# Kernel tuning notes

Hardware: AMD Instinct MI355X
Metric: run time of the kernel (lower is better)

## Reference

```python
import jax, jax.numpy as jnp
import numpy as np

DECAY = 0.99
EPS = 1e-05


def setup_inputs() -> dict:
    key = jax.random.key(0)
    k1, k2 = jax.random.split(key)
    B, C, H, W = 16, 64, 32, 32
    K = 8192
    z_e = jax.random.normal(k1, (B, C, H, W), dtype=jnp.float32)
    embedding = jax.random.normal(k2, (K, C), dtype=jnp.float32)
    cluster_size = jnp.zeros((K,), dtype=jnp.float32)
    embedding_avg = embedding  # initialized as a clone of the codebook
    return {"z_e": z_e, "embedding": embedding, "cluster_size": cluster_size,
            "embedding_avg": embedding_avg}


def reference(z_e, embedding, cluster_size, embedding_avg):
    B, C, H, W = z_e.shape
    K = embedding.shape[0]
    # [N, C] tokens
    z_flat = jnp.transpose(z_e, (0, 2, 3, 1)).reshape(-1, C)
    d = ((z_flat * z_flat).sum(-1, keepdims=True)
         - 2.0 * (z_flat @ embedding.T)
         + (embedding * embedding).sum(-1))
    indices = jnp.argmin(d, axis=1)  # [N] int
    z_q_flat = embedding[indices]    # [N, C]
    z_q = jnp.transpose(z_q_flat.reshape(B, H, W, C), (0, 3, 1, 2))
    # EMA codebook update (training path); one-hot matmuls expressed as segment sums
    counts = jax.ops.segment_sum(jnp.ones(z_flat.shape[0], dtype=z_flat.dtype),
                                 indices, num_segments=K)            # encodings.sum(0)
    dw = jax.ops.segment_sum(z_flat, indices, num_segments=K)        # encodings.T @ z_flat
    new_cluster_size = DECAY * cluster_size + (1.0 - DECAY) * counts
    new_embedding_avg = DECAY * embedding_avg + (1.0 - DECAY) * dw
    n = new_cluster_size.sum()
    cs = (new_cluster_size + EPS) / (n + K * EPS) * n
    new_embedding = new_embedding_avg / cs[:, None]
    # straight-through estimator
    z_q_st = z_e + jax.lax.stop_gradient(z_q - z_e)
    return (z_q_st, indices.reshape(B, H * W), z_q,
            new_embedding, new_cluster_size, new_embedding_avg)
```

## Files before the change

### kernel.cpp

```cpp
#include <hip/hip_runtime.h>

#define DECAYF 0.99f
#define OMDF   0.01f
#define TAU    3.5e-2f

typedef unsigned int u32;
typedef unsigned long long u64;
typedef __attribute__((ext_vector_type(8))) _Float16 f16x8;
typedef __attribute__((ext_vector_type(4))) float f32x4;

#define EN_OFF     0
#define EFRAG_OFF  32768
#define IDX_OFF    32768
#define BEST1_OFF  2129920
#define BEST2_OFF  4227072
#define CNT_OFF    5275648

__device__ __forceinline__ u64 enc_pair(float s, int idx) {
  u32 u = __float_as_uint(s);
  u = (u & 0x80000000u) ? ~u : (u | 0x80000000u);
  return ((u64)u << 32) | (u32)(~idx);
}
__device__ __forceinline__ float dec_score(u64 e) {
  u32 u = (u32)(e >> 32);
  u = (u & 0x80000000u) ? (u & 0x7fffffffu) : ~u;
  return __uint_as_float(u);
}
__device__ __forceinline__ int dec_idx(u64 e) { return (int)(~(u32)e); }
__device__ __forceinline__ unsigned short f2h(float f) {
  union { _Float16 h; unsigned short u; } v;
  v.h = (_Float16)f;
  return v.u;
}
__device__ __forceinline__ float exact_dot(const float* __restrict__ sx,
                                           const float* __restrict__ emb, int k) {
  const float4* e = (const float4*)(emb + (size_t)k * 64);
  float a = 0.f;
#pragma unroll
  for (int q = 0; q < 16; ++q) {
    float4 v = e[q];
    a = fmaf(sx[4 * q],     v.x, a);
    a = fmaf(sx[4 * q + 1], v.y, a);
    a = fmaf(sx[4 * q + 2], v.z, a);
    a = fmaf(sx[4 * q + 3], v.w, a);
  }
  return a;
}

__global__ __launch_bounds__(256) void k_prep(const float* __restrict__ emb,
                                              const float* __restrict__ cs_in,
                                              const float* __restrict__ avg_in,
                                              const float* __restrict__ z_e,
                                              float* __restrict__ en,
                                              unsigned char* __restrict__ efrag,
                                              unsigned char* __restrict__ zfrag,
                                              float* __restrict__ out4,
                                              float* __restrict__ out5,
                                              float* __restrict__ nsum) {
  __shared__ float warr[4];
  __shared__ float sx[64][129];
  int bid = blockIdx.x;
  int t = threadIdx.x;
  if (bid < 512) {
    int tid = bid * 256 + t;
    int k = tid >> 4, q = tid & 15;
    float4 v = ((const float4*)emb)[tid];
    ushort4 hv;
    hv.x = f2h(v.x); hv.y = f2h(v.y); hv.z = f2h(v.z); hv.w = f2h(v.w);
    size_t off = (size_t)(k >> 4) * 2048 + (size_t)(q >> 3) * 1024
               + (size_t)((q >> 1) & 3) * 256 + (size_t)(k & 15) * 16
               + (size_t)(q & 1) * 8;
    *(ushort4*)(efrag + off) = hv;
    float s = v.x * v.x + v.y * v.y + v.z * v.z + v.w * v.w;
    s += __shfl_xor(s, 1, 16);
    s += __shfl_xor(s, 2, 16);
    s += __shfl_xor(s, 4, 16);
    s += __shfl_xor(s, 8, 16);
    if (q == 0) en[k] = 0.5f * s;
  } else if (bid < 1031) {
    int tid = (bid - 512) * 256 + t;
    if (tid < 131072) {
      float4 v = ((const float4*)avg_in)[tid];
      v.x *= DECAYF; v.y *= DECAYF; v.z *= DECAYF; v.w *= DECAYF;
      ((float4*)out5)[tid] = v;
    }
  } else if (bid == 1031) {
    float s = 0.f;
#pragma unroll
    for (int q = 0; q < 8; ++q) {
      int idx = q * 256 + t;
      float4 v = ((const float4*)cs_in)[idx];
      v.x *= DECAYF; v.y *= DECAYF; v.z *= DECAYF; v.w *= DECAYF;
      ((float4*)out4)[idx] = v;
      s += v.x + v.y + v.z + v.w;
    }
    s += __shfl_xor(s, 1, 64);
    s += __shfl_xor(s, 2, 64);
    s += __shfl_xor(s, 4, 64);
    s += __shfl_xor(s, 8, 64);
    s += __shfl_xor(s, 16, 64);
    s += __shfl_xor(s, 32, 64);
    if ((t & 63) == 0) warr[t >> 6] = s;
    __syncthreads();
    if (t == 0) *nsum = warr[0] + warr[1] + warr[2] + warr[3];
  } else {
    int n0 = (bid - 1032) * 128;
    int b = n0 >> 10, hwb = n0 & 1023;
#pragma unroll
    for (int r = 0; r < 8; ++r) {
      int g = r * 256 + t;
      int c = g >> 5, f4 = g & 31;
      float4 v = *(const float4*)(z_e + ((size_t)b << 16) + ((size_t)c << 10)
                                  + hwb + f4 * 4);
      sx[c][f4 * 4 + 0] = v.x;
      sx[c][f4 * 4 + 1] = v.y;
      sx[c][f4 * 4 + 2] = v.z;
      sx[c][f4 * 4 + 3] = v.w;
    }
    __syncthreads();
#pragma unroll
    for (int r = 0; r < 4; ++r) {
      int id = r * 256 + t;
      int nl = id & 127, k = id >> 7;
      int n = n0 + nl;
      unsigned short u[8];
#pragma unroll
      for (int j = 0; j < 8; ++j) u[j] = f2h(sx[k * 8 + j][nl]);
      size_t off = (size_t)(n >> 4) * 2048 + (size_t)(k >> 2) * 1024
                 + (size_t)(k & 3) * 256 + (size_t)(n & 15) * 16;
      *(ushort4*)(zfrag + off)     = make_ushort4(u[0], u[1], u[2], u[3]);
      *(ushort4*)(zfrag + off + 8) = make_ushort4(u[4], u[5], u[6], u[7]);
    }
  }
}

__global__ __launch_bounds__(256) void k_argmin_mfma(
    const unsigned char* __restrict__ zfrag,
    const unsigned char* __restrict__ efrag,
    const float* __restrict__ en, u64* __restrict__ best1,
    float* __restrict__ best2) {
  alignas(16) __shared__ unsigned char sbuf[2][8192];
  __shared__ float sen[512];
  const int tb = blockIdx.x >> 4;
  const int sl = blockIdx.x & 15;
  const int wave = threadIdx.x >> 6, lane = threadIdx.x & 63;
  const int col = lane & 15, g4 = lane >> 4;
  const int token0 = tb * 128 + wave * 32;
  const int scb = sl << 9;

  if (threadIdx.x < 128)
    ((float4*)sen)[threadIdx.x] = ((const float4*)(en + scb))[threadIdx.x];

  f16x8 a[2][2];
  {
    const unsigned char* zb = zfrag + ((size_t)(tb * 8 + wave * 2)) * 2048
                            + (size_t)g4 * 256 + (size_t)col * 16;
    a[0][0] = *(const f16x8*)(zb);
    a[0][1] = *(const f16x8*)(zb + 1024);
    a[1][0] = *(const f16x8*)(zb + 2048);
    a[1][1] = *(const f16x8*)(zb + 3072);
  }
  float b1[8], b2[8];
#pragma unroll
  for (int r = 0; r < 8; ++r) { b1[r] = -3.0e38f; b2[r] = -3.0e38f; }

  const unsigned char* gbase0 = efrag + (size_t)scb * 128;
  auto stage = [&](int ib, int buf) {
    const unsigned char* g = gbase0 + (size_t)ib * 8192 + (size_t)wave * 2048;
#pragma unroll
    for (int it = 0; it < 2; ++it) {
      __builtin_amdgcn_global_load_lds(
          (const __attribute__((address_space(1))) u32*)(g + it * 1024 + lane * 16),
          (__attribute__((address_space(3))) u32*)(&sbuf[buf][wave * 2048 + it * 1024]),
          16, 0, 0);
    }
  };
  stage(0, 0);
  for (int ib = 0; ib < 8; ++ib) {
    __syncthreads();
    if (ib < 7) stage(ib + 1, (ib + 1) & 1);
    const unsigned char* sb0 = &sbuf[ib & 1][0];
#pragma unroll
    for (int ct = 0; ct < 4; ++ct) {
      const int t = ib * 4 + ct;
      const float negen = -sen[t * 16 + col];
      f16x8 bf0 = *(const f16x8*)(sb0 + ct * 2048 + lane * 16);
      f16x8 bf1 = *(const f16x8*)(sb0 + ct * 2048 + 1024 + lane * 16);
      f32x4 acc0, acc1;
#pragma unroll
      for (int r = 0; r < 4; ++r) { acc0[r] = negen; acc1[r] = negen; }
      acc0 = __builtin_amdgcn_mfma_f32_16x16x32_f16(a[0][0], bf0, acc0, 0, 0, 0);
      acc0 = __builtin_amdgcn_mfma_f32_16x16x32_f16(a[0][1], bf1, acc0, 0, 0, 0);
      acc1 = __builtin_amdgcn_mfma_f32_16x16x32_f16(a[1][0], bf0, acc1, 0, 0, 0);
      acc1 = __builtin_amdgcn_mfma_f32_16x16x32_f16(a[1][1], bf1, acc1, 0, 0, 0);
      const u32 emb6 = (u32)(63 - t);
#pragma unroll
      for (int r = 0; r < 4; ++r) {
        float f0 = __uint_as_float((__float_as_uint(acc0[r]) & 0xFFFFFFC0u) | emb6);
        b2[r] = __builtin_amdgcn_fmed3f(f0, b1[r], b2[r]);
        b1[r] = fmaxf(b1[r], f0);
        float f1 = __uint_as_float((__float_as_uint(acc1[r]) & 0xFFFFFFC0u) | emb6);
        b2[4 + r] = __builtin_amdgcn_fmed3f(f1, b1[4 + r], b2[4 + r]);
        b1[4 + r] = fmaxf(b1[4 + r], f1);
      }
    }
  }
  int mi[8];
#pragma unroll
  for (int r = 0; r < 8; ++r) mi[r] = col;
#pragma unroll
  for (int st = 1; st < 16; st <<= 1) {
#pragma unroll
    for (int r = 0; r < 8; ++r) {
      float ob1 = __shfl_xor(b1[r], st, 64);
      float ob2 = __shfl_xor(b2[r], st, 64);
      int omi = __shfl_xor(mi[r], st, 64);
      bool ogt = ob1 > b1[r];
      b2[r] = fmaxf(fminf(b1[r], ob1), fmaxf(b2[r], ob2));
      mi[r] = ogt ? omi : mi[r];
      b1[r] = fmaxf(b1[r], ob1);
    }
  }
  if (col == 0) {
#pragma unroll
    for (int r = 0; r < 8; ++r) {
      int tt = r >> 2, rr = r & 3;
      int token = token0 + tt * 16 + g4 * 4 + rr;
      int t = 63 - (int)(__float_as_uint(b1[r]) & 63u);
      int gcode = scb + t * 16 + mi[r];
      best1[(size_t)sl * 16384 + token] = enc_pair(b1[r], gcode);
      best2[(size_t)sl * 16384 + token] = b2[r];
    }
  }
}

__global__ __launch_bounds__(256) void k_resfix(const float* __restrict__ z_e,
                                                const float* __restrict__ emb,
                                                const float* __restrict__ en,
                                                const u64* __restrict__ best1,
                                                const float* __restrict__ best2,
                                                int* __restrict__ idxa) {
  __shared__ float sxr[64];
  __shared__ int flist[64];
  __shared__ float fth[64];
  __shared__ int nflag;
  __shared__ u32 fmask;
  __shared__ u64 red;
  int t = threadIdx.x;
  int n0 = blockIdx.x * 64;
  if (t == 0) nflag = 0;
  __syncthreads();
  if (t < 64) {
    int n = n0 + t;
    u64 e[16];
#pragma unroll
    for (int s = 0; s < 16; ++s) e[s] = best1[(size_t)s * 16384 + n];
    u64 top = e[0];
#pragma unroll
    for (int s = 1; s < 16; ++s) top = e[s] > top ? e[s] : top;
    float second = -3.0e38f;
#pragma unroll
    for (int s = 0; s < 16; ++s)
      second = fmaxf(second, best2[(size_t)s * 16384 + n]);
#pragma unroll
    for (int s = 0; s < 16; ++s)
      if (e[s] != top) second = fmaxf(second, dec_score(e[s]));
    idxa[n] = dec_idx(top);
    if (dec_score(top) - second < TAU) {
      int p = atomicAdd(&nflag, 1);
      flist[p] = n;
      fth[p] = dec_score(top);
    }
  }
  __syncthreads();
  int nf = nflag;
  for (int i = 0; i < nf; ++i) {
    int n = flist[i];
    float theta = fth[i] - TAU;
    if (t == 0) { fmask = 0; red = 0ull; }
    if (t < 64) {
      sxr[t] = z_e[((size_t)(n >> 10) << 16) + ((size_t)t << 10) + (n & 1023)];
    }
    __syncthreads();
    u64 myb = 0ull;
    if (t < 16) {
      u64 es = best1[(size_t)t * 16384 + n];
      if (best2[(size_t)t * 16384 + n] >= theta) atomicOr(&fmask, 1u << t);
      if (dec_score(es) >= theta) {
        int k = dec_idx(es);
        float a = exact_dot(sxr, emb, k) - en[k];
        myb = enc_pair(a, k);
      }
    }
    __syncthreads();
    u32 fm = fmask;
    while (fm) {
      int s = __ffs(fm) - 1;
      fm &= fm - 1;
      int k0 = (s << 9) + t;
      float a0 = exact_dot(sxr, emb, k0)       - en[k0];
      float a1 = exact_dot(sxr, emb, k0 + 256) - en[k0 + 256];
      u64 m0 = enc_pair(a0, k0), m1 = enc_pair(a1, k0 + 256);
      u64 mm = m0 > m1 ? m0 : m1;
      myb = mm > myb ? mm : myb;
    }
    if (myb) atomicMax(&red, myb);
    __syncthreads();
    if (t == 0) idxa[n] = dec_idx(red);
    __syncthreads();
  }
}

__global__ __launch_bounds__(256) void k_scatter(const float* __restrict__ z_e,
                                                 const int* __restrict__ idxa,
                                                 float* __restrict__ out4,
                                                 float* __restrict__ out5) {
  __shared__ float sx[64][129];
  int t = threadIdx.x;
  int n0 = blockIdx.x * 128;
  int b = n0 >> 10, hwb = n0 & 1023;
#pragma unroll
  for (int r = 0; r < 8; ++r) {
    int g = r * 256 + t;
    int c = g >> 5, f4 = g & 31;
    float4 v = *(const float4*)(z_e + ((size_t)b << 16) + ((size_t)c << 10)
                                + hwb + f4 * 4);
    sx[c][f4 * 4 + 0] = v.x;
    sx[c][f4 * 4 + 1] = v.y;
    sx[c][f4 * 4 + 2] = v.z;
    sx[c][f4 * 4 + 3] = v.w;
  }
  __syncthreads();
  int wave = t >> 6, lane = t & 63;
#pragma unroll
  for (int i = 0; i < 32; ++i) {
    int tok = wave * 32 + i;
    int idx = idxa[n0 + tok];
    atomicAdd(out5 + (size_t)idx * 64 + lane, OMDF * sx[lane][tok]);
    if (lane == 0) atomicAdd(out4 + idx, OMDF);
  }
}

__global__ __launch_bounds__(256) void k_gather(const float* __restrict__ z_e,
                                                const float* __restrict__ emb,
                                                const int* __restrict__ idxa,
                                                float* __restrict__ out0,
                                                float* __restrict__ out1,
                                                float* __restrict__ out2) {
  int tid = blockIdx.x * 256 + threadIdx.x;
  int hw4 = tid & 255;
  int c   = (tid >> 8) & 63;
  int b   = tid >> 14;
  int n0  = (b << 10) + (hw4 << 2);
  size_t off = ((size_t)b << 16) + ((size_t)c << 10) + ((size_t)hw4 << 2);
  float4 z = *(const float4*)(z_e + off);
  int i0 = idxa[n0], i1 = idxa[n0 + 1], i2 = idxa[n0 + 2], i3 = idxa[n0 + 3];
  float4 q;
  q.x = emb[(size_t)i0 * 64 + c];
  q.y = emb[(size_t)i1 * 64 + c];
  q.z = emb[(size_t)i2 * 64 + c];
  q.w = emb[(size_t)i3 * 64 + c];
  float4 st;
  st.x = z.x + (q.x - z.x);
  st.y = z.y + (q.y - z.y);
  st.z = z.z + (q.z - z.z);
  st.w = z.w + (q.w - z.w);
  *(float4*)(out2 + off) = q;
  *(float4*)(out0 + off) = st;
  if (c == 0) {
    float4 f = make_float4((float)i0, (float)i1, (float)i2, (float)i3);
    *(float4*)(out1 + n0) = f;
  }
}

__global__ __launch_bounds__(256) void k_final(const float* __restrict__ out4,
                                               const float* __restrict__ out5,
                                               const float* __restrict__ nsum,
                                               float* __restrict__ out3) {
  int tid = blockIdx.x * 256 + threadIdx.x;
  int k = tid >> 4;
  double nn  = (double)*nsum + 163.84;
  double ncs = (double)out4[k];
  double cs  = (ncs + 1e-5) / (nn + 8192.0 * 1e-5) * nn;
  float inv  = (float)(1.0 / cs);
  float4 v = ((const float4*)out5)[tid];
  v.x *= inv; v.y *= inv; v.z *= inv; v.w *= inv;
  ((float4*)out3)[tid] = v;
}

extern "C" void kernel_launch(void* const* d_in, const int* in_sizes, int n_in,
                              void* d_out, int out_size, void* d_ws, size_t ws_size,
                              hipStream_t stream) {
  const float* z_e    = (const float*)d_in[0];
  const float* emb    = (const float*)d_in[1];
  const float* cs_in  = (const float*)d_in[2];
  const float* avg_in = (const float*)d_in[3];

  float* out  = (float*)d_out;
  float* out0 = out;
  float* out1 = out0 + 1048576;
  float* out2 = out1 + 16384;
  float* out3 = out2 + 1048576;
  float* out4 = out3 + 524288;
  float* out5 = out4 + 8192;

  char* ws = (char*)d_ws;
  float* en            = (float*)(ws + EN_OFF);
  unsigned char* efrag = (unsigned char*)(ws + EFRAG_OFF);
  u64* best1           = (u64*)(ws + BEST1_OFF);
  float* best2         = (float*)(ws + BEST2_OFF);
  int* idxa            = (int*)(ws + IDX_OFF);
  float* nsum          = (float*)(ws + CNT_OFF + 4);
  unsigned char* zfrag = (unsigned char*)out0;

  k_prep       <<<1160, 256, 0, stream>>>(emb, cs_in, avg_in, z_e, en, efrag,
                                          zfrag, out4, out5, nsum);
  k_argmin_mfma<<<2048, 256, 0, stream>>>(zfrag, efrag, en, best1, best2);
  k_resfix     <<<256,  256, 0, stream>>>(z_e, emb, en, best1, best2, idxa);
  k_scatter    <<<128,  256, 0, stream>>>(z_e, idxa, out4, out5);
  k_gather     <<<1024, 256, 0, stream>>>(z_e, emb, idxa, out0, out1, out2);
  k_final      <<<512,  256, 0, stream>>>(out4, out5, nsum, out3);
}
```

Measured before the change: 151.5 us.

## Widen argmin MFMA tile to 64 tokens per wave and flatten scatter kernel

The argmin kernel now has each wave handle 64 tokens, four A fragments, instead of 32. It drops the LDS double-buffered global_load_lds staging and reads codebook fragments straight from global memory into registers with a two-deep software prefetch, so the grid halves. Each B fragment is reused across more MFMAs, at the cost of more registers and no shared LDS reuse across waves. Separately, the scatter kernel is rewritten to use one thread per (token, channel) over 4096 blocks instead of an LDS-transposed 128-block version, which gives more parallelism for the atomics but uses uncoalesced strided z_e reads.

```diff
diff --git a/kernel.cpp b/kernel.cpp
--- a/kernel.cpp
+++ b/kernel.cpp
@@ -139,79 +139,91 @@
     const unsigned char* __restrict__ efrag,
     const float* __restrict__ en, u64* __restrict__ best1,
     float* __restrict__ best2) {
-  alignas(16) __shared__ unsigned char sbuf[2][8192];
   __shared__ float sen[512];
-  const int tb = blockIdx.x >> 4;
   const int sl = blockIdx.x & 15;
   const int wave = threadIdx.x >> 6, lane = threadIdx.x & 63;
+  const int tg = (blockIdx.x >> 4) * 4 + wave;
   const int col = lane & 15, g4 = lane >> 4;
-  const int token0 = tb * 128 + wave * 32;
   const int scb = sl << 9;
 
   if (threadIdx.x < 128)
     ((float4*)sen)[threadIdx.x] = ((const float4*)(en + scb))[threadIdx.x];
-
-  f16x8 a[2][2];
+  __syncthreads();
+
+  f16x8 a[4][2];
   {
-    const unsigned char* zb = zfrag + ((size_t)(tb * 8 + wave * 2)) * 2048
+    const unsigned char* zb = zfrag + (size_t)(tg * 4) * 2048
                             + (size_t)g4 * 256 + (size_t)col * 16;
-    a[0][0] = *(const f16x8*)(zb);
-    a[0][1] = *(const f16x8*)(zb + 1024);
-    a[1][0] = *(const f16x8*)(zb + 2048);
-    a[1][1] = *(const f16x8*)(zb + 3072);
-  }
-  float b1[8], b2[8];
-#pragma unroll
-  for (int r = 0; r < 8; ++r) { b1[r] = -3.0e38f; b2[r] = -3.0e38f; }
-
-  const unsigned char* gbase0 = efrag + (size_t)scb * 128;
-  auto stage = [&](int ib, int buf) {
-    const unsigned char* g = gbase0 + (size_t)ib * 8192 + (size_t)wave * 2048;
-#pragma unroll
-    for (int it = 0; it < 2; ++it) {
-      __builtin_amdgcn_global_load_lds(
-          (const __attribute__((address_space(1))) u32*)(g + it * 1024 + lane * 16),
-          (__attribute__((address_space(3))) u32*)(&sbuf[buf][wave * 2048 + it * 1024]),
-          16, 0, 0);
+#pragma unroll
+    for (int tt = 0; tt < 4; ++tt) {
+      a[tt][0] = *(const f16x8*)(zb + tt * 2048);
+      a[tt][1] = *(const f16x8*)(zb + tt * 2048 + 1024);
+    }
+  }
+  float b1[16], b2[16];
+#pragma unroll
+  for (int r = 0; r < 16; ++r) { b1[r] = -3.0e38f; b2[r] = -3.0e38f; }
+
+  const unsigned char* gb = efrag + (size_t)scb * 128 + (size_t)lane * 16;
+
+  auto body = [&](int t, f16x8 u0, f16x8 u1) {
+    const float negen = -sen[t * 16 + col];
+    f32x4 acc0, acc1, acc2, acc3;
+#pragma unroll
+    for (int r = 0; r < 4; ++r) { acc0[r] = negen; acc1[r] = negen;
+                                  acc2[r] = negen; acc3[r] = negen; }
+    acc0 = __builtin_amdgcn_mfma_f32_16x16x32_f16(a[0][0], u0, acc0, 0, 0, 0);
+    acc1 = __builtin_amdgcn_mfma_f32_16x16x32_f16(a[1][0], u0, acc1, 0, 0, 0);
+    acc2 = __builtin_amdgcn_mfma_f32_16x16x32_f16(a[2][0], u0, acc2, 0, 0, 0);
+    acc3 = __builtin_amdgcn_mfma_f32_16x16x32_f16(a[3][0], u0, acc3, 0, 0, 0);
+    acc0 = __builtin_amdgcn_mfma_f32_16x16x32_f16(a[0][1], u1, acc0, 0, 0, 0);
+    acc1 = __builtin_amdgcn_mfma_f32_16x16x32_f16(a[1][1], u1, acc1, 0, 0, 0);
+    acc2 = __builtin_amdgcn_mfma_f32_16x16x32_f16(a[2][1], u1, acc2, 0, 0, 0);
+    acc3 = __builtin_amdgcn_mfma_f32_16x16x32_f16(a[3][1], u1, acc3, 0, 0, 0);
+    const u32 emb6 = (u32)(63 - t);
+#pragma unroll
+    for (int r = 0; r < 4; ++r) {
+      float f0 = __uint_as_float((__float_as_uint(acc0[r]) & 0xFFFFFFC0u) | emb6);
+      b2[r] = __builtin_amdgcn_fmed3f(f0, b1[r], b2[r]);
+      b1[r] = fmaxf(b1[r], f0);
+      float f1 = __uint_as_float((__float_as_uint(acc1[r]) & 0xFFFFFFC0u) | emb6);
+      b2[4 + r] = __builtin_amdgcn_fmed3f(f1, b1[4 + r], b2[4 + r]);
+      b1[4 + r] = fmaxf(b1[4 + r], f1);
+      float f2 = __uint_as_float((__float_as_uint(acc2[r]) & 0xFFFFFFC0u) | emb6);
+      b2[8 + r] = __builtin_amdgcn_fmed3f(f2, b1[8 + r], b2[8 + r]);
+      b1[8 + r] = fmaxf(b1[8 + r], f2);
+      float f3 = __uint_as_float((__float_as_uint(acc3[r]) & 0xFFFFFFC0u) | emb6);
+      b2[12 + r] = __builtin_amdgcn_fmed3f(f3, b1[12 + r], b2[12 + r]);
+      b1[12 + r] = fmaxf(b1[12 + r], f3);
     }
   };
-  stage(0, 0);
-  for (int ib = 0; ib < 8; ++ib) {
-    __syncthreads();
-    if (ib < 7) stage(ib + 1, (ib + 1) & 1);
-    const unsigned char* sb0 = &sbuf[ib & 1][0];
-#pragma unroll
-    for (int ct = 0; ct < 4; ++ct) {
-      const int t = ib * 4 + ct;
-      const float negen = -sen[t * 16 + col];
-      f16x8 bf0 = *(const f16x8*)(sb0 + ct * 2048 + lane * 16);
-      f16x8 bf1 = *(const f16x8*)(sb0 + ct * 2048 + 1024 + lane * 16);
-      f32x4 acc0, acc1;
-#pragma unroll
-      for (int r = 0; r < 4; ++r) { acc0[r] = negen; acc1[r] = negen; }
-      acc0 = __builtin_amdgcn_mfma_f32_16x16x32_f16(a[0][0], bf0, acc0, 0, 0, 0);
-      acc0 = __builtin_amdgcn_mfma_f32_16x16x32_f16(a[0][1], bf1, acc0, 0, 0, 0);
-      acc1 = __builtin_amdgcn_mfma_f32_16x16x32_f16(a[1][0], bf0, acc1, 0, 0, 0);
-      acc1 = __builtin_amdgcn_mfma_f32_16x16x32_f16(a[1][1], bf1, acc1, 0, 0, 0);
-      const u32 emb6 = (u32)(63 - t);
-#pragma unroll
-      for (int r = 0; r < 4; ++r) {
-        float f0 = __uint_as_float((__float_as_uint(acc0[r]) & 0xFFFFFFC0u) | emb6);
-        b2[r] = __builtin_amdgcn_fmed3f(f0, b1[r], b2[r]);
-        b1[r] = fmaxf(b1[r], f0);
-        float f1 = __uint_as_float((__float_as_uint(acc1[r]) & 0xFFFFFFC0u) | emb6);
-        b2[4 + r] = __builtin_amdgcn_fmed3f(f1, b1[4 + r], b2[4 + r]);
-        b1[4 + r] = fmaxf(b1[4 + r], f1);
-      }
-    }
-  }
-  int mi[8];
-#pragma unroll
-  for (int r = 0; r < 8; ++r) mi[r] = col;
+
+  f16x8 c0 = *(const f16x8*)(gb);
+  f16x8 c1 = *(const f16x8*)(gb + 1024);
+  f16x8 d0 = *(const f16x8*)(gb + 2048);
+  f16x8 d1 = *(const f16x8*)(gb + 3072);
+  for (int t = 0; t < 32; t += 2) {
+    f16x8 u0 = c0, u1 = c1;
+    if (t + 2 < 32) {
+      c0 = *(const f16x8*)(gb + (size_t)(t + 2) * 2048);
+      c1 = *(const f16x8*)(gb + (size_t)(t + 2) * 2048 + 1024);
+    }
+    body(t, u0, u1);
+    u0 = d0; u1 = d1;
+    if (t + 3 < 32) {
+      d0 = *(const f16x8*)(gb + (size_t)(t + 3) * 2048);
+      d1 = *(const f16x8*)(gb + (size_t)(t + 3) * 2048 + 1024);
+    }
+    body(t + 1, u0, u1);
+  }
+
+  int mi[16];
+#pragma unroll
+  for (int r = 0; r < 16; ++r) mi[r] = col;
 #pragma unroll
   for (int st = 1; st < 16; st <<= 1) {
 #pragma unroll
-    for (int r = 0; r < 8; ++r) {
+    for (int r = 0; r < 16; ++r) {
       float ob1 = __shfl_xor(b1[r], st, 64);
       float ob2 = __shfl_xor(b2[r], st, 64);
       int omi = __shfl_xor(mi[r], st, 64);
@@ -223,9 +235,9 @@
   }
   if (col == 0) {
 #pragma unroll
-    for (int r = 0; r < 8; ++r) {
+    for (int r = 0; r < 16; ++r) {
       int tt = r >> 2, rr = r & 3;
-      int token = token0 + tt * 16 + g4 * 4 + rr;
+      int token = tg * 64 + tt * 16 + g4 * 4 + rr;
       int t = 63 - (int)(__float_as_uint(b1[r]) & 63u);
       int gcode = scb + t * 16 + mi[r];
       best1[(size_t)sl * 16384 + token] = enc_pair(b1[r], gcode);
@@ -315,30 +327,13 @@
                                                  const int* __restrict__ idxa,
                                                  float* __restrict__ out4,
                                                  float* __restrict__ out5) {
-  __shared__ float sx[64][129];
-  int t = threadIdx.x;
-  int n0 = blockIdx.x * 128;
-  int b = n0 >> 10, hwb = n0 & 1023;
-#pragma unroll
-  for (int r = 0; r < 8; ++r) {
-    int g = r * 256 + t;
-    int c = g >> 5, f4 = g & 31;
-    float4 v = *(const float4*)(z_e + ((size_t)b << 16) + ((size_t)c << 10)
-                                + hwb + f4 * 4);
-    sx[c][f4 * 4 + 0] = v.x;
-    sx[c][f4 * 4 + 1] = v.y;
-    sx[c][f4 * 4 + 2] = v.z;
-    sx[c][f4 * 4 + 3] = v.w;
-  }
-  __syncthreads();
-  int wave = t >> 6, lane = t & 63;
-#pragma unroll
-  for (int i = 0; i < 32; ++i) {
-    int tok = wave * 32 + i;
-    int idx = idxa[n0 + tok];
-    atomicAdd(out5 + (size_t)idx * 64 + lane, OMDF * sx[lane][tok]);
-    if (lane == 0) atomicAdd(out4 + idx, OMDF);
-  }
+  int tid = blockIdx.x * 256 + threadIdx.x;
+  int n = tid >> 6, c = tid & 63;
+  int idx = idxa[n];
+  int b = n >> 10, hw = n & 1023;
+  float x = z_e[((size_t)b << 16) + ((size_t)c << 10) + hw];
+  atomicAdd(out5 + (size_t)idx * 64 + c, OMDF * x);
+  if (c == 0) atomicAdd(out4 + idx, OMDF);
 }
 
 __global__ __launch_bounds__(256) void k_gather(const float* __restrict__ z_e,
@@ -415,9 +410,9 @@
 
   k_prep       <<<1160, 256, 0, stream>>>(emb, cs_in, avg_in, z_e, en, efrag,
                                           zfrag, out4, out5, nsum);
-  k_argmin_mfma<<<2048, 256, 0, stream>>>(zfrag, efrag, en, best1, best2);
+  k_argmin_mfma<<<1024, 256, 0, stream>>>(zfrag, efrag, en, best1, best2);
   k_resfix     <<<256,  256, 0, stream>>>(z_e, emb, en, best1, best2, idxa);
-  k_scatter    <<<128,  256, 0, stream>>>(z_e, idxa, out4, out5);
+  k_scatter    <<<4096, 256, 0, stream>>>(z_e, idxa, out4, out5);
   k_gather     <<<1024, 256, 0, stream>>>(z_e, emb, idxa, out0, out1, out2);
   k_final      <<<512,  256, 0, stream>>>(out4, out5, nsum, out3);
 }
```

Result: faster. 147.3 us (-2.8%).
